# Kernel optimization log

Measured on AMD Instinct MI355X. Metric: run time of the kernel, lower is better.

Reference implementation:

```python
import jax, jax.numpy as jnp
import numpy as np

EMBED_DIM = 128
ATTN_DIM = 64


def setup_inputs() -> dict:
    key = jax.random.key(0)
    kb, kt, kw1, kb1, kw2, kb2 = jax.random.split(key, 6)
    B, S, E = 2048, 200, EMBED_DIM
    behaviors = jax.random.normal(kb, (B, S, E), dtype=jnp.float32)
    target = jax.random.normal(kt, (B, E), dtype=jnp.float32)
    # Linear params (torch nn.Linear: y = x @ W.T + b); store as [in, out] for einsum
    lim1 = 1.0 / np.sqrt(4 * E)
    W1 = jax.random.uniform(kw1, (4 * E, ATTN_DIM), jnp.float32, -lim1, lim1)
    b1 = jax.random.uniform(kb1, (ATTN_DIM,), jnp.float32, -lim1, lim1)
    lim2 = 1.0 / np.sqrt(ATTN_DIM)
    W2 = jax.random.uniform(kw2, (ATTN_DIM, 1), jnp.float32, -lim2, lim2)
    b2 = jax.random.uniform(kb2, (1,), jnp.float32, -lim2, lim2)
    return {"behaviors": behaviors, "target": target, "W1": W1, "b1": b1, "W2": W2, "b2": b2}


def reference(behaviors, target, W1, b1, W2, b2):
    # behaviors: [B,S,E], target: [B,E] -> broadcast to [B,S,E]
    t = target[:, None, :]  # broadcast instead of repeat
    feat = jnp.concatenate([behaviors,
                            jnp.broadcast_to(t, behaviors.shape),
                            behaviors * t,
                            behaviors - t], axis=-1)  # [B,S,4E]
    h = jax.nn.relu(jnp.einsum('bsf,fa->bsa', feat, W1) + b1)  # [B,S,A]
    w = jax.nn.sigmoid(jnp.einsum('bsa,ao->bso', h, W2) + b2)  # [B,S,1]
    return jnp.sum(w * behaviors, axis=1)  # [B,E]
```

## Files before the change

### kernel.cpp

```cpp
#include <hip/hip_runtime.h>

typedef __attribute__((ext_vector_type(8))) short bf16x8;
typedef __attribute__((ext_vector_type(4))) float f32x4;

__device__ __forceinline__ short f2bf(float f) {
    union { float f; unsigned u; } v; v.f = f;
    unsigned r = (v.u + 0x7FFFu + ((v.u >> 16) & 1u)) >> 16;
    return (short)r;
}

__device__ __forceinline__ float sigmoidf(float x) {
    return 1.0f / (1.0f + __expf(-x));
}

constexpr int S = 200, E = 128, A = 64;
constexpr int NSTRIP = 13;

__device__ __forceinline__ void load_strip(f32x4 av[4][2], const float* __restrict__ bptr,
                                           int st, int l15, int quad)
{
    #pragma unroll
    for (int kt = 0; kt < 4; ++kt) {
        av[kt][0] = f32x4{0.f, 0.f, 0.f, 0.f};
        av[kt][1] = f32x4{0.f, 0.f, 0.f, 0.f};
    }
    const int row = st * 16 + l15;
    if (st < NSTRIP && row < S) {
        const float* rp = bptr + (size_t)row * E + quad * 8;
        #pragma unroll
        for (int kt = 0; kt < 4; ++kt) {
            av[kt][0] = *(const f32x4*)(rp + kt * 32);
            av[kt][1] = *(const f32x4*)(rp + kt * 32 + 4);
        }
    }
}

__global__ __launch_bounds__(256, 4) void attn_fused(
    const float* __restrict__ behaviors,
    const float* __restrict__ target,
    const float* __restrict__ W1,
    const float* __restrict__ b1,
    const float* __restrict__ W2,
    const float* __restrict__ b2,
    float* __restrict__ out)
{
    __shared__ short wb_f[16 * 512];
    __shared__ short wbtmp[E * A];
    __shared__ float red[4 * 128];
    __shared__ float t_lds[E];
    __shared__ float bias_lds[A];
    __shared__ float w2_lds[A];

    const int tid  = threadIdx.x;
    const int bat  = blockIdx.x;
    const int lane = tid & 63;
    const int wave = tid >> 6;
    const int l15  = lane & 15;
    const int quad = lane >> 4;

    const float* bptr = behaviors + (size_t)bat * S * E;

    f32x4 avA[4][2], avB[4][2];
    load_strip(avA, bptr, wave, l15, quad);

    if (tid < E) t_lds[tid] = target[(size_t)bat * E + tid];
    __syncthreads();

    for (int i = tid; i < E * A; i += 256) {
        const int e = i >> 6, a = i & 63;
        wbtmp[i] = f2bf(W1[e * A + a] + W1[(384 + e) * A + a]
                        + t_lds[e] * W1[(256 + e) * A + a]);
    }
    {
        const int a = tid & 63, seg = tid >> 6;
        float acc = 0.f;
        #pragma unroll 8
        for (int e = seg * 32; e < seg * 32 + 32; ++e)
            acc += t_lds[e] * (W1[(128 + e) * A + a] - W1[(384 + e) * A + a]);
        red[seg * 64 + a] = acc;
    }
    __syncthreads();
    if (tid < A) {
        bias_lds[tid] = b1[tid] + red[tid] + red[64 + tid] + red[128 + tid] + red[192 + tid];
        w2_lds[tid] = W2[tid];
    }
    for (int i = tid; i < E * A; i += 256) {
        const int j = i & 7, ln = (i >> 3) & 63, f = i >> 9;
        const int kt = f >> 2, nt = f & 3;
        const int n = nt * 16 + (ln & 15);
        const int k = kt * 32 + (ln >> 4) * 8 + j;
        wb_f[i] = wbtmp[k * A + n];
    }
    __syncthreads();

    float bias_l[4], w2_l[4];
    #pragma unroll
    for (int nt = 0; nt < 4; ++nt) {
        bias_l[nt] = bias_lds[nt * 16 + l15];
        w2_l[nt]   = w2_lds[nt * 16 + l15];
    }
    const float b2v = b2[0];

    f32x4 oacc[4][2];
    #pragma unroll
    for (int kt = 0; kt < 4; ++kt) {
        oacc[kt][0] = f32x4{0.f, 0.f, 0.f, 0.f};
        oacc[kt][1] = f32x4{0.f, 0.f, 0.f, 0.f};
    }

    #pragma unroll
    for (int it = 0; it < 4; ++it) {
        const int st = wave + it * 4;
        if (st >= NSTRIP) break;
        f32x4 (*cur)[2] = (it & 1) ? avB : avA;
        f32x4 (*nxt)[2] = (it & 1) ? avA : avB;
        load_strip(nxt, bptr, st + 4, l15, quad);

        f32x4 acc[4];
        #pragma unroll
        for (int nt = 0; nt < 4; ++nt) acc[nt] = f32x4{0.f, 0.f, 0.f, 0.f};

        #pragma unroll
        for (int kt = 0; kt < 4; ++kt) {
            bf16x8 af;
            #pragma unroll
            for (int h = 0; h < 2; ++h)
                #pragma unroll
                for (int c = 0; c < 4; ++c)
                    af[h * 4 + c] = f2bf(cur[kt][h][c]);
            #pragma unroll
            for (int nt = 0; nt < 4; ++nt) {
                bf16x8 bf1 = *(const bf16x8*)&wb_f[(kt * 4 + nt) * 512 + lane * 8];
                acc[nt] = __builtin_amdgcn_mfma_f32_16x16x32_bf16(af, bf1, acc[nt], 0, 0, 0);
            }
        }

        float wgt[4];
        #pragma unroll
        for (int reg = 0; reg < 4; ++reg) {
            float p = 0.f;
            #pragma unroll
            for (int nt = 0; nt < 4; ++nt) {
                const float h = acc[nt][reg] + bias_l[nt];
                p += fmaxf(h, 0.f) * w2_l[nt];
            }
            p += __shfl_xor(p, 1, 64);
            p += __shfl_xor(p, 2, 64);
            p += __shfl_xor(p, 4, 64);
            p += __shfl_xor(p, 8, 64);
            wgt[reg] = sigmoidf(p + b2v);
        }

        const int srcl = (l15 >> 2) << 4;
        const float t0 = __shfl(wgt[0], srcl, 64);
        const float t1 = __shfl(wgt[1], srcl, 64);
        const float t2 = __shfl(wgt[2], srcl, 64);
        const float t3 = __shfl(wgt[3], srcl, 64);
        const float wl = (l15 & 2) ? ((l15 & 1) ? t3 : t2)
                                   : ((l15 & 1) ? t1 : t0);

        #pragma unroll
        for (int kt = 0; kt < 4; ++kt)
            #pragma unroll
            for (int h = 0; h < 2; ++h) {
                oacc[kt][h][0] += wl * cur[kt][h][0];
                oacc[kt][h][1] += wl * cur[kt][h][1];
                oacc[kt][h][2] += wl * cur[kt][h][2];
                oacc[kt][h][3] += wl * cur[kt][h][3];
            }
    }

    #pragma unroll
    for (int kt = 0; kt < 4; ++kt)
        #pragma unroll
        for (int h = 0; h < 2; ++h)
            #pragma unroll
            for (int c = 0; c < 4; ++c) {
                float v = oacc[kt][h][c];
                v += __shfl_xor(v, 1, 64);
                v += __shfl_xor(v, 2, 64);
                v += __shfl_xor(v, 4, 64);
                v += __shfl_xor(v, 8, 64);
                oacc[kt][h][c] = v;
            }

    if (l15 == 0) {
        #pragma unroll
        for (int kt = 0; kt < 4; ++kt) {
            *(f32x4*)&red[wave * 128 + kt * 32 + quad * 8]     = oacc[kt][0];
            *(f32x4*)&red[wave * 128 + kt * 32 + quad * 8 + 4] = oacc[kt][1];
        }
    }
    __syncthreads();
    if (tid < E) {
        out[(size_t)bat * E + tid] =
            red[tid] + red[128 + tid] + red[256 + tid] + red[384 + tid];
    }
}

extern "C" void kernel_launch(void* const* d_in, const int* in_sizes, int n_in,
                              void* d_out, int out_size, void* d_ws, size_t ws_size,
                              hipStream_t stream) {
    const float* behaviors = (const float*)d_in[0];
    const float* target    = (const float*)d_in[1];
    const float* W1        = (const float*)d_in[2];
    const float* b1        = (const float*)d_in[3];
    const float* W2        = (const float*)d_in[4];
    const float* b2        = (const float*)d_in[5];
    float* out = (float*)d_out;

    hipLaunchKernelGGL(attn_fused, dim3(2048), dim3(256), 0, stream,
                       behaviors, target, W1, b1, W2, b2, out);
}
```

Baseline: 353.2 us.

## Split per-batch weight folding into a prep kernel and stream weights via workspace

Moves the per-batch folding of W1 with the target vector (bf16 weight fragments plus folded bias) into a separate prep kernel that writes to workspace. The main kernel then loads the pre-swizzled fragments with vector loads and issues two strips of behavior loads up front, so the weight setup no longer sits on its critical path. It also converts fp32 to bf16 with the packed v_cvt_pk_bf16_f32 instruction. In exchange the prep kernel writes and the main kernel reads about 32 MB of weight fragments through global memory, and there is an extra launch; a fallback fused kernel runs when the workspace is too small.

```diff
diff --git a/kernel.cpp b/kernel.cpp
--- a/kernel.cpp
+++ b/kernel.cpp
@@ -35,7 +35,199 @@
     }
 }
 
-__global__ __launch_bounds__(256, 4) void attn_fused(
+__device__ __forceinline__ bf16x8 pack8(const f32x4 a, const f32x4 b) {
+    union { bf16x8 v; unsigned u[4]; } r;
+    asm("v_cvt_pk_bf16_f32 %0, %1, %2" : "=v"(r.u[0]) : "v"(a[0]), "v"(a[1]));
+    asm("v_cvt_pk_bf16_f32 %0, %1, %2" : "=v"(r.u[1]) : "v"(a[2]), "v"(a[3]));
+    asm("v_cvt_pk_bf16_f32 %0, %1, %2" : "=v"(r.u[2]) : "v"(b[0]), "v"(b[1]));
+    asm("v_cvt_pk_bf16_f32 %0, %1, %2" : "=v"(r.u[3]) : "v"(b[2]), "v"(b[3]));
+    return r.v;
+}
+
+__global__ __launch_bounds__(256, 4) void attn_prep(
+    const float* __restrict__ target,
+    const float* __restrict__ W1,
+    const float* __restrict__ b1,
+    short* __restrict__ wb_all,
+    float* __restrict__ beta_all)
+{
+    __shared__ float wtmp[E * 65];
+    __shared__ float redp[256];
+    __shared__ float t_lds[E];
+
+    const int tid = threadIdx.x;
+    const int bat = blockIdx.x;
+
+    if (tid < E) t_lds[tid] = target[(size_t)bat * E + tid];
+    __syncthreads();
+
+    for (int i = tid; i < E * A; i += 256) {
+        const int e = i >> 6;
+        wtmp[e * 65 + (i & 63)] =
+            W1[i] + W1[3 * E * A + i] + t_lds[e] * W1[2 * E * A + i];
+    }
+    {
+        const int a = tid & 63, seg = tid >> 6;
+        float acc = 0.f;
+        #pragma unroll 8
+        for (int e = seg * 32; e < seg * 32 + 32; ++e)
+            acc += t_lds[e] * (W1[(128 + e) * A + a] - W1[(384 + e) * A + a]);
+        redp[seg * 64 + a] = acc;
+    }
+    __syncthreads();
+    if (tid < A)
+        beta_all[(size_t)bat * A + tid] =
+            b1[tid] + redp[tid] + redp[64 + tid] + redp[128 + tid] + redp[192 + tid];
+
+    short* wbd = wb_all + (size_t)bat * (E * A);
+    for (int i = tid; i < E * A; i += 256) {
+        const int j = i & 7, ln = (i >> 3) & 63, f = i >> 9;
+        const int kt = f >> 2, nt = f & 3;
+        const int n = nt * 16 + (ln & 15);
+        const int k = kt * 32 + (ln >> 4) * 8 + j;
+        wbd[i] = f2bf(wtmp[k * 65 + n]);
+    }
+}
+
+__global__ __launch_bounds__(256, 4) void attn_main(
+    const float* __restrict__ behaviors,
+    const float* __restrict__ W2,
+    const float* __restrict__ b2,
+    const short* __restrict__ wb_all,
+    const float* __restrict__ beta_all,
+    float* __restrict__ out)
+{
+    __shared__ short wb_f[16 * 512];
+    __shared__ float red[4 * 128];
+    __shared__ float bias_lds[A];
+    __shared__ float w2_lds[A];
+
+    const int tid  = threadIdx.x;
+    const int bat  = blockIdx.x;
+    const int lane = tid & 63;
+    const int wave = tid >> 6;
+    const int l15  = lane & 15;
+    const int quad = lane >> 4;
+
+    const float* bptr = behaviors + (size_t)bat * S * E;
+
+    f32x4 avA[4][2], avB[4][2];
+    load_strip(avA, bptr, wave, l15, quad);
+    load_strip(avB, bptr, wave + 4, l15, quad);
+
+    {
+        const f32x4* wsrc = (const f32x4*)(wb_all + (size_t)bat * (E * A));
+        #pragma unroll
+        for (int i = 0; i < 4; ++i)
+            *(f32x4*)&wb_f[(tid + i * 256) * 8] = wsrc[tid + i * 256];
+    }
+    if (tid < A) {
+        bias_lds[tid] = beta_all[(size_t)bat * A + tid];
+        w2_lds[tid]   = W2[tid];
+    }
+    __syncthreads();
+
+    float bias_l[4], w2_l[4];
+    #pragma unroll
+    for (int nt = 0; nt < 4; ++nt) {
+        bias_l[nt] = bias_lds[nt * 16 + l15];
+        w2_l[nt]   = w2_lds[nt * 16 + l15];
+    }
+    const float b2v = b2[0];
+
+    f32x4 oacc[4][2];
+    #pragma unroll
+    for (int kt = 0; kt < 4; ++kt) {
+        oacc[kt][0] = f32x4{0.f, 0.f, 0.f, 0.f};
+        oacc[kt][1] = f32x4{0.f, 0.f, 0.f, 0.f};
+    }
+
+    #pragma unroll
+    for (int it = 0; it < 4; ++it) {
+        const int st = wave + it * 4;
+        if (st >= NSTRIP) break;
+        f32x4 (*cur)[2] = (it & 1) ? avB : avA;
+
+        f32x4 acc[4];
+        #pragma unroll
+        for (int nt = 0; nt < 4; ++nt) acc[nt] = f32x4{0.f, 0.f, 0.f, 0.f};
+
+        #pragma unroll
+        for (int kt = 0; kt < 4; ++kt) {
+            const bf16x8 af = pack8(cur[kt][0], cur[kt][1]);
+            #pragma unroll
+            for (int nt = 0; nt < 4; ++nt) {
+                bf16x8 bf1 = *(const bf16x8*)&wb_f[(kt * 4 + nt) * 512 + lane * 8];
+                acc[nt] = __builtin_amdgcn_mfma_f32_16x16x32_bf16(af, bf1, acc[nt], 0, 0, 0);
+            }
+        }
+
+        float wgt[4];
+        #pragma unroll
+        for (int reg = 0; reg < 4; ++reg) {
+            float p = 0.f;
+            #pragma unroll
+            for (int nt = 0; nt < 4; ++nt) {
+                const float h = acc[nt][reg] + bias_l[nt];
+                p += fmaxf(h, 0.f) * w2_l[nt];
+            }
+            p += __shfl_xor(p, 1, 64);
+            p += __shfl_xor(p, 2, 64);
+            p += __shfl_xor(p, 4, 64);
+            p += __shfl_xor(p, 8, 64);
+            wgt[reg] = sigmoidf(p + b2v);
+        }
+
+        const int srcl = (l15 >> 2) << 4;
+        const float t0 = __shfl(wgt[0], srcl, 64);
+        const float t1 = __shfl(wgt[1], srcl, 64);
+        const float t2 = __shfl(wgt[2], srcl, 64);
+        const float t3 = __shfl(wgt[3], srcl, 64);
+        const float wl = (l15 & 2) ? ((l15 & 1) ? t3 : t2)
+                                   : ((l15 & 1) ? t1 : t0);
+
+        #pragma unroll
+        for (int kt = 0; kt < 4; ++kt)
+            #pragma unroll
+            for (int h = 0; h < 2; ++h) {
+                oacc[kt][h][0] += wl * cur[kt][h][0];
+                oacc[kt][h][1] += wl * cur[kt][h][1];
+                oacc[kt][h][2] += wl * cur[kt][h][2];
+                oacc[kt][h][3] += wl * cur[kt][h][3];
+            }
+
+        if (st + 8 < NSTRIP) load_strip(cur, bptr, st + 8, l15, quad);
+    }
+
+    #pragma unroll
+    for (int kt = 0; kt < 4; ++kt)
+        #pragma unroll
+        for (int h = 0; h < 2; ++h)
+            #pragma unroll
+            for (int c = 0; c < 4; ++c) {
+                float v = oacc[kt][h][c];
+                v += __shfl_xor(v, 1, 64);
+                v += __shfl_xor(v, 2, 64);
+                v += __shfl_xor(v, 4, 64);
+                v += __shfl_xor(v, 8, 64);
+                oacc[kt][h][c] = v;
+            }
+
+    if (l15 == 0) {
+        #pragma unroll
+        for (int kt = 0; kt < 4; ++kt) {
+            *(f32x4*)&red[wave * 128 + kt * 32 + quad * 8]     = oacc[kt][0];
+            *(f32x4*)&red[wave * 128 + kt * 32 + quad * 8 + 4] = oacc[kt][1];
+        }
+    }
+    __syncthreads();
+    if (tid < E) {
+        out[(size_t)bat * E + tid] =
+            red[tid] + red[128 + tid] + red[256 + tid] + red[384 + tid];
+    }
+}
+
+__global__ __launch_bounds__(256, 4) void attn_fused_fb(
     const float* __restrict__ behaviors,
     const float* __restrict__ target,
     const float* __restrict__ W1,
@@ -209,6 +401,18 @@
     const float* b2        = (const float*)d_in[5];
     float* out = (float*)d_out;
 
-    hipLaunchKernelGGL(attn_fused, dim3(2048), dim3(256), 0, stream,
-                       behaviors, target, W1, b1, W2, b2, out);
-}
+    const size_t wb_bytes   = (size_t)2048 * (E * A) * sizeof(short);
+    const size_t beta_bytes = (size_t)2048 * A * sizeof(float);
+
+    if (d_ws && ws_size >= wb_bytes + beta_bytes) {
+        short* wb_all   = (short*)d_ws;
+        float* beta_all = (float*)((char*)d_ws + wb_bytes);
+        hipLaunchKernelGGL(attn_prep, dim3(2048), dim3(256), 0, stream,
+                           target, W1, b1, wb_all, beta_all);
+        hipLaunchKernelGGL(attn_main, dim3(2048), dim3(256), 0, stream,
+                           behaviors, W2, b2, wb_all, beta_all, out);
+    } else {
+        hipLaunchKernelGGL(attn_fused_fb, dim3(2048), dim3(256), 0, stream,
+                           behaviors, target, W1, b1, W2, b2, out);
+    }
+}
```

Measured after the change: 368.2 us. 4.3% more time.
